# Optimization experiments

Measured on AMD Instinct MI355X. Metric: run time of the kernel, lower is better.

Reference implementation:

```python
import jax, jax.numpy as jnp
import numpy as np

N_NODES = 50000
N_EDGES = 1600000
IN_CH = 128
HID_CH = 128


def setup_inputs() -> dict:
    key = jax.random.key(0)
    ks = jax.random.split(key, 8)
    node_embed = jax.random.normal(ks[0], (N_NODES, IN_CH), dtype=jnp.float32)
    node_pos = jax.random.normal(ks[1], (N_NODES, 3), dtype=jnp.float32)
    edge_index = jax.random.randint(ks[2], (2, N_EDGES), 0, N_NODES, dtype=jnp.int64)
    # Linear weights stored as [in, out] so y = x @ W + b (matches torch x @ W.T + b)
    W_res = jax.random.normal(ks[3], (IN_CH, HID_CH), dtype=jnp.float32) / np.sqrt(IN_CH)
    W_msg = jax.random.normal(ks[4], (2 * IN_CH + 1, HID_CH), dtype=jnp.float32) / np.sqrt(2 * IN_CH + 1)
    b_msg = jax.random.normal(ks[5], (HID_CH,), dtype=jnp.float32) * 0.01
    W_upd = jax.random.normal(ks[6], (IN_CH + HID_CH, HID_CH), dtype=jnp.float32) / np.sqrt(IN_CH + HID_CH)
    b_upd = jax.random.normal(ks[7], (HID_CH,), dtype=jnp.float32) * 0.01
    return {"node_embed": node_embed, "node_pos": node_pos, "edge_index": edge_index,
            "W_res": W_res, "W_msg": W_msg, "b_msg": b_msg, "W_upd": W_upd, "b_upd": b_upd}


def reference(node_embed, node_pos, edge_index, W_res, W_msg, b_msg, W_upd, b_upd):
    row, col = edge_index[0], edge_index[1]
    # squared distance per edge: [E, 1]
    diff = node_pos[row] - node_pos[col]
    dist = jnp.sum(diff * diff, axis=1, keepdims=True)
    # message MLP on concat(src, tgt, dist): [E, 2*in+1] -> [E, hidden]
    msg_in = jnp.concatenate([node_embed[row], node_embed[col], dist], axis=-1)
    msg = jax.nn.relu(msg_in @ W_msg + b_msg)
    # scatter-sum messages into target nodes (index = col, as in original)
    aggr = jax.ops.segment_sum(msg, col, num_segments=N_NODES)
    upd_in = jnp.concatenate([node_embed, aggr], axis=-1)
    new_node_embed = node_embed @ W_res + jax.nn.relu(upd_in @ W_upd + b_upd)
    return new_node_embed
```

## Files before the change

kernel.cpp:

```cpp
#include <hip/hip_runtime.h>
#include <hip/hip_bf16.h>
#include <cstdint>


typedef __bf16 bf16x8 __attribute__((ext_vector_type(8)));
typedef float floatx4 __attribute__((ext_vector_type(4)));
typedef float floatx2 __attribute__((ext_vector_type(2)));
typedef unsigned int uintx4 __attribute__((ext_vector_type(4)));

#define NBINS 1024
#define NCPY 8
#define BINF_CAP 320
#define CAP_OUT 2816
#define CUR_STRIDE 32

__device__ __forceinline__ ushort f2bf(float f) {
  union { float f; uint i; } v; v.f = f;
  uint r = v.i + 0x7fff + ((v.i >> 16) & 1);
  return (ushort)(r >> 16);
}
__device__ __forceinline__ bf16x8 load_frag(const ushort* p) {
  uint4 v = *(const uint4*)p;
  return __builtin_bit_cast(bf16x8, v);
}
__device__ __forceinline__ floatx2 pmax0(floatx2 a) {
#if __has_builtin(__builtin_elementwise_max)
  return __builtin_elementwise_max(a, (floatx2)(0.f));
#else
  floatx2 r; r.x = fmaxf(a.x, 0.f); r.y = fmaxf(a.y, 0.f); return r;
#endif
}
__device__ __forceinline__ floatx2 cvtpk2(uint qu) {
#if __has_builtin(__builtin_amdgcn_cvt_pk_f32_fp8)
  return __builtin_amdgcn_cvt_pk_f32_fp8((int)qu, false);
#else
  floatx2 o = {__builtin_amdgcn_cvt_f32_fp8((int)qu, 0),
               __builtin_amdgcn_cvt_f32_fp8((int)qu, 1)};
  return o;
#endif
}

struct WSrc { const float* s[5]; };

__global__ __launch_bounds__(256) void k01_cast_bin(
    const float* __restrict__ embed, ushort* __restrict__ Eb, int n4, int nb_cast,
    WSrc ws, ushort* __restrict__ Wt,
    const int* __restrict__ ei, int E,
    uint* __restrict__ bin_cursor, uint* __restrict__ binned, int bb)
{
  __shared__ uint hist[NBINS];
  __shared__ uint sbase[NBINS];
  __shared__ uint lcur[NBINS];

  if ((int)blockIdx.x >= bb) {
    int cb = blockIdx.x - bb;
    if (cb < nb_cast) {
      int i = cb * 256 + threadIdx.x;
      if (i < n4) {
        float4 v = ((const float4*)embed)[i];
        ushort4 o;
        o.x = f2bf(v.x); o.y = f2bf(v.y); o.z = f2bf(v.z); o.w = f2bf(v.w);
        ((ushort4*)Eb)[i] = o;
      }
      return;
    }
    int wb = cb - nb_cast;
    const float* s = ws.s[wb];
    ushort* d = Wt + wb * 16384;
    for (int i = threadIdx.x; i < 16384; i += 256) {
      int k = i >> 7, n = i & 127;
      d[n * 128 + k] = f2bf(s[i]);
    }
    return;
  }

  const int t = threadIdx.x;
#pragma unroll
  for (int k = 0; k < NBINS / 256; ++k) hist[t + k * 256] = 0;
  __syncthreads();

  const int e0 = blockIdx.x * 2048 + t * 8;
  int rr[8], cc[8];
  bool any = (e0 < E);
  if (any) {
    int4 r0 = ((const int4*)(ei + e0))[0];
    int4 r1 = ((const int4*)(ei + e0))[1];
    int4 c0 = ((const int4*)(ei + E + e0))[0];
    int4 c1 = ((const int4*)(ei + E + e0))[1];
    rr[0]=r0.x; rr[1]=r0.y; rr[2]=r0.z; rr[3]=r0.w;
    rr[4]=r1.x; rr[5]=r1.y; rr[6]=r1.z; rr[7]=r1.w;
    cc[0]=c0.x; cc[1]=c0.y; cc[2]=c0.z; cc[3]=c0.w;
    cc[4]=c1.x; cc[5]=c1.y; cc[6]=c1.z; cc[7]=c1.w;
#pragma unroll
    for (int j = 0; j < 8; ++j) {
      if (e0 + j < E) atomicAdd(&hist[cc[j] >> 6], 1u);
    }
  }
  __syncthreads();
  const int cpy = blockIdx.x & 7;
  uint* cur = bin_cursor + (size_t)cpy * NBINS * CUR_STRIDE;
#pragma unroll
  for (int k = 0; k < NBINS / 256; ++k) {
    int b2 = t + k * 256;
    uint h = hist[b2];
    sbase[b2] = h ? atomicAdd(cur + (size_t)b2 * CUR_STRIDE, h) : 0u;
    lcur[b2] = 0;
  }
  __syncthreads();
  uint* mybin = binned + (size_t)cpy * NBINS * BINF_CAP;
  if (any) {
#pragma unroll
    for (int j = 0; j < 8; ++j) {
      if (e0 + j < E) {
        int b = cc[j] >> 6;
        uint ofs = atomicAdd(&lcur[b], 1u);
        uint idx = sbase[b] + ofs;
        if (idx < BINF_CAP)
          mybin[(size_t)b * BINF_CAP + idx] = ((uint)cc[j] << 16) | (uint)rr[j];
      }
    }
  }
}

__global__ __launch_bounds__(256) void k2_proj_sort(
    const ushort* __restrict__ Ab, int M, int rt,
    const ushort* __restrict__ W1t, const ushort* __restrict__ W2t,
    const float* __restrict__ b_msg, const float* __restrict__ pos,
    unsigned char* __restrict__ P1, ushort* __restrict__ P2b,
    const uint* __restrict__ bin_cursor, const uint* __restrict__ binned,
    uint* __restrict__ sorted, int* __restrict__ nstart, int* __restrict__ ncnt)
{
  __shared__ ushort sdist[NCPY * BINF_CAP];
  __shared__ uint   srt[CAP_OUT];
  __shared__ float  spos[64 * 3];
  __shared__ uint   h64[64], st64[64], lc64[64];
  __shared__ uint   ccnt[NCPY];
  __shared__ uint   stot;

  if ((int)blockIdx.x >= rt) {
    const int bin = blockIdx.x - rt;
    const int col0 = bin * 64;
    const int ncol = min(64, M - col0);
    const int tid = threadIdx.x;

    if (tid < 64) { h64[tid] = 0; lc64[tid] = 0; }
    if (tid < NCPY)
      ccnt[tid] = min(bin_cursor[((size_t)tid * NBINS + bin) * CUR_STRIDE],
                      (uint)BINF_CAP);
    for (int i = tid; i < ncol * 3; i += 256) spos[i] = pos[(size_t)col0 * 3 + i];
    __syncthreads();

    for (int c = 0; c < NCPY; ++c) {
      const int cnt = (int)ccnt[c];
      const uint* src = binned + ((size_t)c * NBINS + bin) * BINF_CAP;
      for (int i = tid; i < cnt; i += 256) {
        uint rc = src[i];
        uint row = rc & 0xffffu, c6 = (rc >> 16) & 63u;
        float dx = spos[c6 * 3 + 0] - pos[(size_t)row * 3 + 0];
        float dy = spos[c6 * 3 + 1] - pos[(size_t)row * 3 + 1];
        float dz = spos[c6 * 3 + 2] - pos[(size_t)row * 3 + 2];
        sdist[c * BINF_CAP + i] = f2bf(dx * dx + dy * dy + dz * dz);
        atomicAdd(&h64[c6], 1u);
      }
    }
    __syncthreads();

    if (tid == 0) {
      uint run = 0;
      for (int c = 0; c < 64; ++c) { st64[c] = run; run += (h64[c] + 3u) & ~3u; }
      stot = min(run, (uint)CAP_OUT);
    }
    __syncthreads();

    for (int c = 0; c < NCPY; ++c) {
      const int cnt = (int)ccnt[c];
      const uint* src = binned + ((size_t)c * NBINS + bin) * BINF_CAP;
      for (int i = tid; i < cnt; i += 256) {
        uint rc = src[i];
        uint c6 = (rc >> 16) & 63u;
        uint p = st64[c6] + atomicAdd(&lc64[c6], 1u);
        if (p < CAP_OUT)
          srt[p] = ((rc & 0xffffu) << 16) | (uint)sdist[c * BINF_CAP + i];
      }
    }
    __syncthreads();

    const size_t obase = (size_t)bin * CAP_OUT;
    for (int i = tid; i < (int)stot; i += 256)
      sorted[obase + i] = srt[i];
    if (tid < ncol) {
      nstart[col0 + tid] = (int)(obase + st64[tid]);
      ncnt[col0 + tid] = (int)h64[tid];
    }
    return;
  }

  const int wv = threadIdx.x >> 6, lane = threadIdx.x & 63;
  const int q = lane >> 4, lr = lane & 15;
  const int m0 = blockIdx.x * 32;
  const int n0 = wv * 32;

  const ushort* Wt2[2] = {W1t, W2t};
  bf16x8 bfr[2][2][4];
#pragma unroll
  for (int ws = 0; ws < 2; ++ws)
#pragma unroll
    for (int nt = 0; nt < 2; ++nt) {
      int colc = n0 + nt * 16 + lr;
#pragma unroll
      for (int kc = 0; kc < 4; ++kc)
        bfr[ws][nt][kc] = load_frag(Wt2[ws] + colc * 128 + kc * 32 + q * 8);
    }

  floatx4 z = {0.f, 0.f, 0.f, 0.f};
  floatx4 acc[2][2][2];
#pragma unroll
  for (int ws = 0; ws < 2; ++ws)
#pragma unroll
    for (int mt = 0; mt < 2; ++mt)
#pragma unroll
      for (int nt = 0; nt < 2; ++nt) acc[ws][mt][nt] = z;

  const int r0 = min(m0 + lr, M - 1);
  const int r1 = min(m0 + 16 + lr, M - 1);
#pragma unroll
  for (int kc = 0; kc < 4; ++kc) {
    bf16x8 a0 = load_frag(Ab + (size_t)r0 * 128 + kc * 32 + q * 8);
    bf16x8 a1 = load_frag(Ab + (size_t)r1 * 128 + kc * 32 + q * 8);
#pragma unroll
    for (int ws = 0; ws < 2; ++ws)
#pragma unroll
      for (int nt = 0; nt < 2; ++nt) {
        acc[ws][0][nt] = __builtin_amdgcn_mfma_f32_16x16x32_bf16(a0, bfr[ws][nt][kc], acc[ws][0][nt], 0, 0, 0);
        acc[ws][1][nt] = __builtin_amdgcn_mfma_f32_16x16x32_bf16(a1, bfr[ws][nt][kc], acc[ws][1][nt], 0, 0, 0);
      }
  }

#pragma unroll
  for (int nt = 0; nt < 2; ++nt) {
    int colc = n0 + nt * 16 + lr;
    float bias = b_msg[colc];
#pragma unroll
    for (int mt = 0; mt < 2; ++mt)
#pragma unroll
      for (int i = 0; i < 4; ++i) {
        int r = m0 + mt * 16 + q * 4 + i;
        if (r < M) {
          int p8 = __builtin_amdgcn_cvt_pk_fp8_f32(acc[0][mt][nt][i], 0.f, 0, false);
          P1[(size_t)r * 128 + colc] = (unsigned char)(p8 & 0xff);
          P2b[(size_t)r * 128 + colc] = f2bf(acc[1][mt][nt][i] + bias);
        }
      }
  }
}

__global__ __launch_bounds__(256) void aggregate(const int* __restrict__ ncnt,
                                                 const int* __restrict__ nstart,
                                                 const uint* __restrict__ sorted,
                                                 const unsigned char* __restrict__ P1,
                                                 const ushort* __restrict__ P2b,
                                                 const float* __restrict__ wd,
                                                 ushort* __restrict__ aggr, int M)
{
  const int lane = threadIdx.x & 63;
  const int ch = lane * 2;
  const int wid = blockIdx.x * 4 + (threadIdx.x >> 6);
  const int nw = gridDim.x * 4;

  float2 wl = *(const float2*)(wd + ch);
  floatx2 wv = {wl.x, wl.y};

  for (int n = wid; n < M; n += nw) {
    uint p2u = *(const uint*)(P2b + (size_t)n * 128 + ch);
    floatx2 p2 = {__int_as_float((int)(p2u << 16)),
                  __int_as_float((int)(p2u & 0xffff0000u))};

    const int cnt = ncnt[n];
    const uint* base = sorted + nstart[n];

    floatx2 accA = {0.f, 0.f}, accB = {0.f, 0.f};

    auto edge = [&](uint rec, floatx2& acc) {
      float d = __int_as_float((int)(rec << 16));
      uint off = ((rec >> 9) & 0x007fff80u) | (uint)ch;
      uint qu = (uint)*(const ushort*)(P1 + off);
#if __has_builtin(__builtin_elementwise_fma)
      floatx2 u = __builtin_elementwise_fma((floatx2)(d), wv, p2);
#else
      floatx2 u = (floatx2)(d) * wv + p2;
#endif
      floatx2 t = cvtpk2(qu) + u;
      acc += pmax0(t);
    };

    int i = 0;
    for (; i + 8 <= cnt; i += 8) {
      uintx4 ra = __builtin_nontemporal_load((const uintx4*)(base + i));
      uintx4 rb = __builtin_nontemporal_load((const uintx4*)(base + i + 4));
      edge(ra.x, accA); edge(ra.y, accB); edge(ra.z, accA); edge(ra.w, accB);
      edge(rb.x, accA); edge(rb.y, accB); edge(rb.z, accA); edge(rb.w, accB);
    }
    for (; i < cnt; ++i) edge(base[i], accA);

    floatx2 acc = accA + accB;
    uint o = (uint)f2bf(acc.x) | ((uint)f2bf(acc.y) << 16);
    *(uint*)(aggr + (size_t)n * 128 + ch) = o;
  }
}

__global__ __launch_bounds__(256) void gemm_upd_mfma(
    const ushort* __restrict__ Eb, const ushort* __restrict__ Gb, int M,
    const ushort* __restrict__ Wu1t, const ushort* __restrict__ Wu2t,
    const ushort* __restrict__ Wrt, const float* __restrict__ b_upd,
    float* __restrict__ out)
{
  const int wv = threadIdx.x >> 6, lane = threadIdx.x & 63;
  const int q = lane >> 4, lr = lane & 15;
  const int m0 = blockIdx.x * 32;
  const int n0 = wv * 32;

  bf16x8 b1[2][4], b2[2][4], br[2][4];
#pragma unroll
  for (int nt = 0; nt < 2; ++nt) {
    int colc = n0 + nt * 16 + lr;
#pragma unroll
    for (int kc = 0; kc < 4; ++kc) {
      b1[nt][kc] = load_frag(Wu1t + colc * 128 + kc * 32 + q * 8);
      b2[nt][kc] = load_frag(Wu2t + colc * 128 + kc * 32 + q * 8);
      br[nt][kc] = load_frag(Wrt  + colc * 128 + kc * 32 + q * 8);
    }
  }

  floatx4 z = {0.f, 0.f, 0.f, 0.f};
  floatx4 acc_u[2][2], acc_r[2][2];
#pragma unroll
  for (int mt = 0; mt < 2; ++mt)
#pragma unroll
    for (int nt = 0; nt < 2; ++nt) { acc_u[mt][nt] = z; acc_r[mt][nt] = z; }

  const int r0 = min(m0 + lr, M - 1);
  const int r1 = min(m0 + 16 + lr, M - 1);
#pragma unroll
  for (int kc = 0; kc < 4; ++kc) {
    bf16x8 ae0 = load_frag(Eb + (size_t)r0 * 128 + kc * 32 + q * 8);
    bf16x8 ae1 = load_frag(Eb + (size_t)r1 * 128 + kc * 32 + q * 8);
    bf16x8 ag0 = load_frag(Gb + (size_t)r0 * 128 + kc * 32 + q * 8);
    bf16x8 ag1 = load_frag(Gb + (size_t)r1 * 128 + kc * 32 + q * 8);
#pragma unroll
    for (int nt = 0; nt < 2; ++nt) {
      acc_u[0][nt] = __builtin_amdgcn_mfma_f32_16x16x32_bf16(ae0, b1[nt][kc], acc_u[0][nt], 0, 0, 0);
      acc_u[1][nt] = __builtin_amdgcn_mfma_f32_16x16x32_bf16(ae1, b1[nt][kc], acc_u[1][nt], 0, 0, 0);
      acc_u[0][nt] = __builtin_amdgcn_mfma_f32_16x16x32_bf16(ag0, b2[nt][kc], acc_u[0][nt], 0, 0, 0);
      acc_u[1][nt] = __builtin_amdgcn_mfma_f32_16x16x32_bf16(ag1, b2[nt][kc], acc_u[1][nt], 0, 0, 0);
      acc_r[0][nt] = __builtin_amdgcn_mfma_f32_16x16x32_bf16(ae0, br[nt][kc], acc_r[0][nt], 0, 0, 0);
      acc_r[1][nt] = __builtin_amdgcn_mfma_f32_16x16x32_bf16(ae1, br[nt][kc], acc_r[1][nt], 0, 0, 0);
    }
  }

#pragma unroll
  for (int nt = 0; nt < 2; ++nt) {
    int colc = n0 + nt * 16 + lr;
    float bias = b_upd[colc];
#pragma unroll
    for (int mt = 0; mt < 2; ++mt)
#pragma unroll
      for (int i = 0; i < 4; ++i) {
        int r = m0 + mt * 16 + q * 4 + i;
        if (r < M)
          out[(size_t)r * 128 + colc] = acc_r[mt][nt][i] + fmaxf(acc_u[mt][nt][i] + bias, 0.f);
      }
  }
}

extern "C" void kernel_launch(void* const* d_in, const int* in_sizes, int n_in,
                              void* d_out, int out_size, void* d_ws, size_t ws_size,
                              hipStream_t stream)
{
  const float* embed = (const float*)d_in[0];
  const float* pos   = (const float*)d_in[1];
  const int*   ei    = (const int*)d_in[2];
  const float* W_res = (const float*)d_in[3];
  const float* W_msg = (const float*)d_in[4];
  const float* b_msg = (const float*)d_in[5];
  const float* W_upd = (const float*)d_in[6];
  const float* b_upd = (const float*)d_in[7];
  float* out = (float*)d_out;

  const int M = in_sizes[0] / 128;
  const int E = in_sizes[2] / 2;

  ushort* Eb = (ushort*)d_ws;
  unsigned char* P1f8 = (unsigned char*)(Eb + (size_t)M * 128);
  ushort* P2b = (ushort*)(P1f8 + (size_t)M * 128);
  ushort* Gb  = P2b + (size_t)M * 128;
  ushort* Wt  = Gb  + (size_t)M * 128;
  uint*   binned = (uint*)(Wt + 5 * 16384);
  uint*   sorted = binned + (size_t)NCPY * NBINS * BINF_CAP;
  int*    nstart = (int*)(sorted + (size_t)NBINS * CAP_OUT);
  int*    ncnt   = nstart + M;
  uint*   bin_cursor = (uint*)(ncnt + M);

  (void)hipMemsetAsync(bin_cursor, 0,
                       (size_t)NCPY * NBINS * CUR_STRIDE * sizeof(uint), stream);

  WSrc wsrc;
  wsrc.s[0] = W_msg;
  wsrc.s[1] = W_msg + 128 * 128;
  wsrc.s[2] = W_res;
  wsrc.s[3] = W_upd;
  wsrc.s[4] = W_upd + 128 * 128;

  int n4 = M * 128 / 4;
  int nb_cast = (n4 + 255) / 256;
  int bb = (E + 2047) / 2048;
  k01_cast_bin<<<bb + nb_cast + 5, 256, 0, stream>>>(
      embed, Eb, n4, nb_cast, wsrc, Wt, ei, E, bin_cursor, binned, bb);

  int rt = (M + 31) / 32;
  int nb2 = (M + 63) / 64;
  k2_proj_sort<<<rt + nb2, 256, 0, stream>>>(
      Eb, M, rt, Wt, Wt + 16384, b_msg, pos, P1f8, P2b,
      bin_cursor, binned, sorted, nstart, ncnt);

  int ab = min((M + 3) / 4, 2048);
  aggregate<<<ab, 256, 0, stream>>>(ncnt, nstart, sorted, P1f8, P2b,
                                    W_msg + 256 * 128, Gb, M);

  gemm_upd_mfma<<<rt, 256, 0, stream>>>(Eb, Gb, M, Wt + 3 * 16384, Wt + 4 * 16384,
                                        Wt + 2 * 16384, b_upd, out);
}
```

Measured before the change: 268.8 us.

## Process more edges and cast elements per block in binning kernel

Each binning block now handles 8192 edges instead of 2048, so far fewer global cursor atomics are issued per bin. The col indices are read twice, once for the histogram and once for scattering. Cast blocks now process 8 float4 per thread, and the per-bin capacity grows to 384 to absorb larger per-block chunks. The trade-off is extra index reads, fewer blocks (less parallelism), and a larger binned buffer.

```diff
diff --git a/kernel.cpp b/kernel.cpp
--- a/kernel.cpp
+++ b/kernel.cpp
@@ -10,9 +10,10 @@
 
 #define NBINS 1024
 #define NCPY 8
-#define BINF_CAP 320
+#define BINF_CAP 384
 #define CAP_OUT 2816
 #define CUR_STRIDE 32
+#define EPB 8192
 
 __device__ __forceinline__ ushort f2bf(float f) {
   union { float f; uint i; } v; v.f = f;
@@ -55,12 +56,16 @@
   if ((int)blockIdx.x >= bb) {
     int cb = blockIdx.x - bb;
     if (cb < nb_cast) {
-      int i = cb * 256 + threadIdx.x;
-      if (i < n4) {
-        float4 v = ((const float4*)embed)[i];
-        ushort4 o;
-        o.x = f2bf(v.x); o.y = f2bf(v.y); o.z = f2bf(v.z); o.w = f2bf(v.w);
-        ((ushort4*)Eb)[i] = o;
+      int base = cb * 2048 + threadIdx.x;
+#pragma unroll
+      for (int k = 0; k < 8; ++k) {
+        int i = base + k * 256;
+        if (i < n4) {
+          float4 v = ((const float4*)embed)[i];
+          ushort4 o;
+          o.x = f2bf(v.x); o.y = f2bf(v.y); o.z = f2bf(v.z); o.w = f2bf(v.w);
+          ((ushort4*)Eb)[i] = o;
+        }
       }
       return;
     }
@@ -79,24 +84,23 @@
   for (int k = 0; k < NBINS / 256; ++k) hist[t + k * 256] = 0;
   __syncthreads();
 
-  const int e0 = blockIdx.x * 2048 + t * 8;
-  int rr[8], cc[8];
-  bool any = (e0 < E);
-  if (any) {
-    int4 r0 = ((const int4*)(ei + e0))[0];
-    int4 r1 = ((const int4*)(ei + e0))[1];
-    int4 c0 = ((const int4*)(ei + E + e0))[0];
-    int4 c1 = ((const int4*)(ei + E + e0))[1];
-    rr[0]=r0.x; rr[1]=r0.y; rr[2]=r0.z; rr[3]=r0.w;
-    rr[4]=r1.x; rr[5]=r1.y; rr[6]=r1.z; rr[7]=r1.w;
-    cc[0]=c0.x; cc[1]=c0.y; cc[2]=c0.z; cc[3]=c0.w;
-    cc[4]=c1.x; cc[5]=c1.y; cc[6]=c1.z; cc[7]=c1.w;
-#pragma unroll
-    for (int j = 0; j < 8; ++j) {
-      if (e0 + j < E) atomicAdd(&hist[cc[j] >> 6], 1u);
+  const int blk0 = blockIdx.x * EPB;
+#pragma unroll
+  for (int c = 0; c < EPB / 2048; ++c) {
+    int e0 = blk0 + c * 2048 + t * 8;
+    if (e0 < E) {
+      int4 c0 = ((const int4*)(ei + E + e0))[0];
+      int4 c1 = ((const int4*)(ei + E + e0))[1];
+      int cc[8];
+      cc[0]=c0.x; cc[1]=c0.y; cc[2]=c0.z; cc[3]=c0.w;
+      cc[4]=c1.x; cc[5]=c1.y; cc[6]=c1.z; cc[7]=c1.w;
+#pragma unroll
+      for (int j = 0; j < 8; ++j)
+        if (e0 + j < E) atomicAdd(&hist[cc[j] >> 6], 1u);
     }
   }
   __syncthreads();
+
   const int cpy = blockIdx.x & 7;
   uint* cur = bin_cursor + (size_t)cpy * NBINS * CUR_STRIDE;
 #pragma unroll
@@ -107,16 +111,30 @@
     lcur[b2] = 0;
   }
   __syncthreads();
+
   uint* mybin = binned + (size_t)cpy * NBINS * BINF_CAP;
-  if (any) {
-#pragma unroll
-    for (int j = 0; j < 8; ++j) {
-      if (e0 + j < E) {
-        int b = cc[j] >> 6;
-        uint ofs = atomicAdd(&lcur[b], 1u);
-        uint idx = sbase[b] + ofs;
-        if (idx < BINF_CAP)
-          mybin[(size_t)b * BINF_CAP + idx] = ((uint)cc[j] << 16) | (uint)rr[j];
+#pragma unroll
+  for (int c = 0; c < EPB / 2048; ++c) {
+    int e0 = blk0 + c * 2048 + t * 8;
+    if (e0 < E) {
+      int4 r0 = ((const int4*)(ei + e0))[0];
+      int4 r1 = ((const int4*)(ei + e0))[1];
+      int4 c0 = ((const int4*)(ei + E + e0))[0];
+      int4 c1 = ((const int4*)(ei + E + e0))[1];
+      int rr[8], cc[8];
+      rr[0]=r0.x; rr[1]=r0.y; rr[2]=r0.z; rr[3]=r0.w;
+      rr[4]=r1.x; rr[5]=r1.y; rr[6]=r1.z; rr[7]=r1.w;
+      cc[0]=c0.x; cc[1]=c0.y; cc[2]=c0.z; cc[3]=c0.w;
+      cc[4]=c1.x; cc[5]=c1.y; cc[6]=c1.z; cc[7]=c1.w;
+#pragma unroll
+      for (int j = 0; j < 8; ++j) {
+        if (e0 + j < E) {
+          int b = cc[j] >> 6;
+          uint ofs = atomicAdd(&lcur[b], 1u);
+          uint idx = sbase[b] + ofs;
+          if (idx < BINF_CAP)
+            mybin[(size_t)b * BINF_CAP + idx] = ((uint)cc[j] << 16) | (uint)rr[j];
+        }
       }
     }
   }
@@ -411,8 +429,8 @@
   wsrc.s[4] = W_upd + 128 * 128;
 
   int n4 = M * 128 / 4;
-  int nb_cast = (n4 + 255) / 256;
-  int bb = (E + 2047) / 2048;
+  int nb_cast = (n4 + 2047) / 2048;
+  int bb = (E + EPB - 1) / EPB;
   k01_cast_bin<<<bb + nb_cast + 5, 256, 0, stream>>>(
       embed, Eb, n4, nb_cast, wsrc, Wt, ei, E, bin_cursor, binned, bb);
 
```

Measured after the change: 239.5 us. 10.9% less time.
